# Kernel optimization log

Hardware: AMD Instinct MI355X
Metric: run time of the kernel (lower is better)

The kernel has to match this reference:

```python
import jax, jax.numpy as jnp
import numpy as np

BATCH, PAST_N, HID, FEAT = 256, 512, 512, 1
INIT_MULT = 0.01  # ones * 0.01 initial state (perturb_init=False / eval mode)


def setup_inputs() -> dict:
    key = jax.random.key(0)
    ks = jax.random.split(key, 8)
    s = 1.0 / np.sqrt(HID)
    return {
        "input_seq": jax.random.normal(ks[0], (BATCH, PAST_N, FEAT), dtype=jnp.float32),
        "future_n": 64,
        "W_ih": jax.random.uniform(ks[1], (4 * HID, FEAT), minval=-s, maxval=s, dtype=jnp.float32),
        "W_hh": jax.random.uniform(ks[2], (4 * HID, HID), minval=-s, maxval=s, dtype=jnp.float32),
        "b_ih": jax.random.uniform(ks[3], (4 * HID,), minval=-s, maxval=s, dtype=jnp.float32),
        "b_hh": jax.random.uniform(ks[4], (4 * HID,), minval=-s, maxval=s, dtype=jnp.float32),
        "W_dec": jax.random.uniform(ks[5], (FEAT, HID), minval=-s, maxval=s, dtype=jnp.float32),
        "b_dec": jax.random.uniform(ks[6], (FEAT,), minval=-s, maxval=s, dtype=jnp.float32),
    }


def _lstm_cell(x, h, c, W_ih, W_hh, b_ih, b_hh):
    # PyTorch LSTMCell: gates ordered (i, f, g, o)
    gates = x @ W_ih.T + b_ih + h @ W_hh.T + b_hh  # [B, 4H]
    i, f, g, o = jnp.split(gates, 4, axis=-1)
    c_new = jax.nn.sigmoid(f) * c + jax.nn.sigmoid(i) * jnp.tanh(g)
    h_new = jax.nn.sigmoid(o) * jnp.tanh(c_new)
    return h_new, c_new


def reference(input_seq, future_n, W_ih, W_hh, b_ih, b_hh, W_dec, b_dec):
    B, T, _ = input_seq.shape
    h0 = jnp.full((B, HID), INIT_MULT, dtype=input_seq.dtype)
    c0 = jnp.full((B, HID), INIT_MULT, dtype=input_seq.dtype)

    xs = jnp.swapaxes(input_seq, 0, 1)  # [T, B, F]

    def past_step(carry, x_t):
        h, c = carry
        h, c = _lstm_cell(x_t, h, c, W_ih, W_hh, b_ih, b_hh)
        return (h, c), h

    (h, c), past_h = jax.lax.scan(past_step, (h0, c0), xs)  # past_h: [T, B, H]

    def future_step(carry, _):
        h, c = carry
        x_t = h @ W_dec.T + b_dec  # decode hidden -> next input, [B, F]
        h, c = _lstm_cell(x_t, h, c, W_ih, W_hh, b_ih, b_hh)
        return (h, c), h

    _, fut_h = jax.lax.scan(future_step, (h, c), None, length=future_n)  # [F_n, B, H]

    all_h = jnp.concatenate([past_h, fut_h], axis=0)  # [T+F_n, B, H]
    all_h = jnp.swapaxes(all_h, 0, 1)  # [B, T+F_n, H]
    return all_h @ W_dec.T + b_dec  # [B, T+F_n, 1]
```

## Files before the change

kernel.cpp:

```cpp
#include <hip/hip_runtime.h>
#include <hip/hip_fp16.h>


#define TPAST 512
#define TTOT  576
#define HIDN  512
#define BW    16
#define HW    64
#define NGRP  8
#define NTHR  512
#define HSTR  520
#define HSTR64 130
#define GSTR  261
#define BATCHN 256

typedef _Float16 half8   __attribute__((ext_vector_type(8)));
typedef _Float16 half2v  __attribute__((ext_vector_type(2)));
typedef float    float4v __attribute__((ext_vector_type(4)));

__device__ __forceinline__ float fast_exp(float x) {
    return __builtin_amdgcn_exp2f(x * 1.44269504f);
}
__device__ __forceinline__ float fast_sigmoid(float x) {
    return __builtin_amdgcn_rcpf(1.0f + fast_exp(-x));
}
__device__ __forceinline__ float fast_tanh(float x) {
    return 1.0f - 2.0f * __builtin_amdgcn_rcpf(fast_exp(2.0f * x) + 1.0f);
}

__global__ __launch_bounds__(NTHR, 1)
void lstm_forecast_kernel(const float* __restrict__ xseq,
                          const float* __restrict__ Wih,
                          const float* __restrict__ Whh,
                          const float* __restrict__ bih,
                          const float* __restrict__ bhh,
                          const float* __restrict__ Wdec,
                          const float* __restrict__ bdec,
                          float* __restrict__ out,
                          unsigned int* __restrict__ flagbase,
                          unsigned int* __restrict__ hbuf)
{
    __shared__ _Float16 hcur[BW * HSTR];
    __shared__ float    gates[BW * GSTR];
    __shared__ float    wdecs[HIDN];
    __shared__ float    xcur[BW];

    const int tid  = threadIdx.x;
    const int bb   = blockIdx.x & 15;
    const int gb   = blockIdx.x >> 4;
    const int lane = tid & 63;
    const int wave = tid >> 6;
    const int m    = lane & 15;
    const int q    = lane >> 4;

    half8 Wf[2][16];
    {
        #pragma unroll
        for (int cbi = 0; cbi < 2; ++cbi) {
            const int col = (2 * wave + cbi) * 16 + m;
            const int gt  = col >> 6;
            const int jl  = col & 63;
            const float* wr = Whh + (size_t)(gt * HIDN + gb * HW + jl) * HIDN;
            #pragma unroll
            for (int kk = 0; kk < 16; ++kk) {
                const int k0 = kk * 32 + q * 8;
                float4v u = *(const float4v*)(wr + k0);
                float4v v = *(const float4v*)(wr + k0 + 4);
                half8 h;
                h[0] = (_Float16)u[0]; h[1] = (_Float16)u[1];
                h[2] = (_Float16)u[2]; h[3] = (_Float16)u[3];
                h[4] = (_Float16)v[0]; h[5] = (_Float16)v[1];
                h[6] = (_Float16)v[2]; h[7] = (_Float16)v[3];
                Wf[cbi][kk] = h;
            }
        }
    }

    const int eb = tid >> 5;
    const int jj = tid & 31;
    const int j0 = 2 * jj;
    float wih_r[2][4], bsum_r[2][4], wd[2];
    #pragma unroll
    for (int p = 0; p < 2; ++p) {
        const int jg = gb * HW + j0 + p;
        #pragma unroll
        for (int gt = 0; gt < 4; ++gt) {
            const int r = gt * HIDN + jg;
            wih_r[p][gt]  = Wih[r];
            bsum_r[p][gt] = bih[r] + bhh[r];
        }
        wd[p] = Wdec[jg];
    }
    const float bdecv = bdec[0];
    float c0 = 0.01f, c1 = 0.01f;

    {
        const _Float16 hinit = (_Float16)0.01f;
        for (int i = tid; i < BW * HSTR; i += NTHR) hcur[i] = hinit;
        wdecs[tid] = Wdec[tid];
        if (tid < BW) xcur[tid] = xseq[(bb * BW + tid) * TPAST + 0];
    }
    __syncthreads();

    unsigned int* gflags = flagbase + bb * 16;
    const int bglob_e = bb * BW + eb;
    const bool dp_lead = ((lane & 31) == 0);
    float dpv = 0.f;

    for (int t = 0; t < TTOT; ++t) {
        float4v acc0 = {0.f, 0.f, 0.f, 0.f};
        float4v acc1 = {0.f, 0.f, 0.f, 0.f};
        const _Float16* arow = hcur + m * HSTR + q * 8;
        #pragma unroll
        for (int kk = 0; kk < 16; ++kk) {
            half8 af = *(const half8*)(arow + kk * 32);
            acc0 = __builtin_amdgcn_mfma_f32_16x16x32_f16(af, Wf[0][kk], acc0, 0, 0, 0);
            acc1 = __builtin_amdgcn_mfma_f32_16x16x32_f16(af, Wf[1][kk], acc1, 0, 0, 0);
        }
        {
            const int colbase = wave * 32;
            #pragma unroll
            for (int r = 0; r < 4; ++r) {
                gates[(q * 4 + r) * GSTR + colbase +      m] = acc0[r];
                gates[(q * 4 + r) * GSTR + colbase + 16 + m] = acc1[r];
            }
        }
        const int tn = t + 1;
        float xq = 0.f;
        if (tn < TPAST && tid < BW) xq = xseq[(bb * BW + tid) * TPAST + tn];

        __syncthreads();

        {
            const float xc = xcur[eb];
            const float* grow = gates + eb * GSTR;

            float gi = grow[       j0] + xc * wih_r[0][0] + bsum_r[0][0];
            float gf = grow[ 64  + j0] + xc * wih_r[0][1] + bsum_r[0][1];
            float gg = grow[128  + j0] + xc * wih_r[0][2] + bsum_r[0][2];
            float go = grow[192  + j0] + xc * wih_r[0][3] + bsum_r[0][3];
            c0 = fast_sigmoid(gf) * c0 + fast_sigmoid(gi) * fast_tanh(gg);
            const float h0 = fast_sigmoid(go) * fast_tanh(c0);

            gi = grow[       j0 + 1] + xc * wih_r[1][0] + bsum_r[1][0];
            gf = grow[ 64  + j0 + 1] + xc * wih_r[1][1] + bsum_r[1][1];
            gg = grow[128  + j0 + 1] + xc * wih_r[1][2] + bsum_r[1][2];
            go = grow[192  + j0 + 1] + xc * wih_r[1][3] + bsum_r[1][3];
            c1 = fast_sigmoid(gf) * c1 + fast_sigmoid(gi) * fast_tanh(gg);
            const float h1 = fast_sigmoid(go) * fast_tanh(c1);

            half2v hp; hp[0] = (_Float16)h0; hp[1] = (_Float16)h1;
            const unsigned int bits = __builtin_bit_cast(unsigned int, hp);
            unsigned int* hdst = hbuf
                + (size_t)((tn & 1) * BATCHN + bglob_e) * (HIDN / 2)
                + gb * (HW / 2) + jj;
            __hip_atomic_store(hdst, bits, __ATOMIC_RELAXED,
                               __HIP_MEMORY_SCOPE_AGENT);

            float dp = h0 * wd[0] + h1 * wd[1];
            dp += __shfl_down(dp, 16);
            dp += __shfl_down(dp, 8);
            dp += __shfl_down(dp, 4);
            dp += __shfl_down(dp, 2);
            dp += __shfl_down(dp, 1);
            dpv = dp;
        }

        __syncthreads();

        if (t == TTOT - 1) {
            if (dp_lead)
                atomicAdd(out + bglob_e * TTOT + t,
                          dpv + (gb == 0 ? bdecv : 0.0f));
            break;
        }

        const unsigned int target = (unsigned int)tn;
        if (tid == 0)
            __hip_atomic_store(gflags + gb, target, __ATOMIC_RELAXED,
                               __HIP_MEMORY_SCOPE_AGENT);
        {
            const unsigned int* slot = gflags + (lane & 7);
            int guard = 0;
            for (;;) {
                const unsigned int v = __hip_atomic_load(
                    slot, __ATOMIC_RELAXED, __HIP_MEMORY_SCOPE_AGENT);
                if (__ballot(v >= target) == ~0ull) break;
                __builtin_amdgcn_s_sleep(1);
                if (++guard > (1 << 22)) break;
            }
        }
        __builtin_amdgcn_sched_barrier(0);

        {
            const int p1 = tn & 1;
            const unsigned long long* hsrc = (const unsigned long long*)hbuf
                + (size_t)(p1 * BATCHN + bb * BW) * (HIDN / 4);
            unsigned long long* hc64 = (unsigned long long*)hcur;
            #pragma unroll
            for (int i = 0; i < 4; ++i) {
                const int idx = lane + 64 * i;
                const int row = 2 * wave + (idx >> 7);
                const int col = idx & 127;
                hc64[row * HSTR64 + col] =
                    __hip_atomic_load(hsrc + row * (HIDN / 4) + col,
                                      __ATOMIC_RELAXED, __HIP_MEMORY_SCOPE_AGENT);
            }
        }
        __syncthreads();

        if (dp_lead)
            atomicAdd(out + bglob_e * TTOT + t,
                      dpv + (gb == 0 ? bdecv : 0.0f));
        if (tn >= TPAST) {
            const _Float16* hr = hcur + eb * HSTR + jj * 16;
            const float*    wr = wdecs + jj * 16;
            float dx = 0.f;
            #pragma unroll
            for (int u = 0; u < 2; ++u) {
                half8 hv = *(const half8*)(hr + u * 8);
                #pragma unroll
                for (int e = 0; e < 8; ++e)
                    dx += (float)hv[e] * wr[u * 8 + e];
            }
            dx += __shfl_down(dx, 16);
            dx += __shfl_down(dx, 8);
            dx += __shfl_down(dx, 4);
            dx += __shfl_down(dx, 2);
            dx += __shfl_down(dx, 1);
            if (dp_lead) xcur[eb] = dx + bdecv;
        } else {
            if (tid < BW) xcur[tid] = xq;
        }
    }
}

extern "C" void kernel_launch(void* const* d_in, const int* in_sizes, int n_in,
                              void* d_out, int out_size, void* d_ws, size_t ws_size,
                              hipStream_t stream) {
    (void)in_sizes; (void)n_in; (void)ws_size;
    const float* xseq = (const float*)d_in[0];
    const float* Wih  = (const float*)d_in[2];
    const float* Whh  = (const float*)d_in[3];
    const float* bih  = (const float*)d_in[4];
    const float* bhh  = (const float*)d_in[5];
    const float* Wdec = (const float*)d_in[6];
    const float* bdec = (const float*)d_in[7];
    float* out = (float*)d_out;

    unsigned int* flags = (unsigned int*)d_ws;
    unsigned int* hbuf  = (unsigned int*)((char*)d_ws + 8192);

    hipMemsetAsync(d_ws, 0, 8192, stream);
    hipMemsetAsync(d_out, 0, (size_t)out_size * sizeof(float), stream);
    lstm_forecast_kernel<<<dim3(128), dim3(NTHR), 0, stream>>>(
        xseq, Wih, Whh, bih, bhh, Wdec, bdec, out, flags, hbuf);
}
```

Before: 1.968 ms.

## Use sc0 cache-bypass loads/stores for inter-block sync with runtime validation

Replaces the agent-scope atomic loads and stores used for the cross-block hidden-state exchange and step flags with inline-asm global loads and stores carrying the sc0 bit. At startup each block group runs a token handshake to confirm that these accesses see each other's writes, and keeps the original atomic path as a fallback if any block fails. The aim is lower latency per recurrent step on the sync and h-exchange path. The cost is a one-time prologue handshake, an extra vmcnt drain before each step's barrier, and reliance on cache-coherence behaviour that the handshake checks at runtime rather than the memory model guaranteeing.

```diff
diff --git a/kernel.cpp b/kernel.cpp
--- a/kernel.cpp
+++ b/kernel.cpp
@@ -28,6 +28,29 @@
     return 1.0f - 2.0f * __builtin_amdgcn_rcpf(fast_exp(2.0f * x) + 1.0f);
 }
 
+__device__ __forceinline__ void st_sc0(unsigned int* p, unsigned int v) {
+    asm volatile("global_store_dword %0, %1, off sc0" :: "v"(p), "v"(v) : "memory");
+}
+__device__ __forceinline__ unsigned int ld_sc0(const unsigned int* p) {
+    unsigned int v;
+    asm volatile("global_load_dword %0, %1, off sc0\n\ts_waitcnt vmcnt(0)"
+                 : "=v"(v) : "v"(p) : "memory");
+    return v;
+}
+__device__ __forceinline__ void ld4_sc0(const unsigned long long* p,
+                                        unsigned long long& a, unsigned long long& b,
+                                        unsigned long long& c, unsigned long long& d) {
+    asm volatile("global_load_dwordx2 %0, %4, off sc0\n\t"
+                 "global_load_dwordx2 %1, %4, off offset:512 sc0\n\t"
+                 "global_load_dwordx2 %2, %4, off offset:1024 sc0\n\t"
+                 "global_load_dwordx2 %3, %4, off offset:1536 sc0\n\t"
+                 "s_waitcnt vmcnt(0)"
+                 : "=v"(a), "=v"(b), "=v"(c), "=v"(d) : "v"(p) : "memory");
+}
+__device__ __forceinline__ void drain_vm() {
+    asm volatile("s_waitcnt vmcnt(0)" ::: "memory");
+}
+
 __global__ __launch_bounds__(NTHR, 1)
 void lstm_forecast_kernel(const float* __restrict__ xseq,
                           const float* __restrict__ Wih,
@@ -37,13 +60,14 @@
                           const float* __restrict__ Wdec,
                           const float* __restrict__ bdec,
                           float* __restrict__ out,
-                          unsigned int* __restrict__ flagbase,
+                          unsigned int* __restrict__ ws32,
                           unsigned int* __restrict__ hbuf)
 {
     __shared__ _Float16 hcur[BW * HSTR];
     __shared__ float    gates[BW * GSTR];
     __shared__ float    wdecs[HIDN];
     __shared__ float    xcur[BW];
+    __shared__ int      vfast_s;
 
     const int tid  = threadIdx.x;
     const int bb   = blockIdx.x & 15;
@@ -52,6 +76,11 @@
     const int wave = tid >> 6;
     const int m    = lane & 15;
     const int q    = lane >> 4;
+
+    unsigned int* gflags  = ws32 + bb * 16;
+    unsigned int* vflags  = ws32 + 1024 / 4 + bb * 16;
+    unsigned int* okflags = ws32 + 2048 / 4 + bb * 16;
+    unsigned int* tokens  = ws32 + 3072 / 4;
 
     half8 Wf[2][16];
     {
@@ -100,9 +129,57 @@
         wdecs[tid] = Wdec[tid];
         if (tid < BW) xcur[tid] = xseq[(bb * BW + tid) * TPAST + 0];
     }
+
+    if (wave == 0) {
+        unsigned int okacc = 1;
+        for (int r = 0; r < 3; ++r) {
+            if (lane == 0) {
+                st_sc0(tokens + (bb * 8 + gb) * 16, (unsigned)(r * 16 + gb + 1));
+                drain_vm();
+                __hip_atomic_store(vflags + gb, (unsigned)(r + 1),
+                                   __ATOMIC_RELAXED, __HIP_MEMORY_SCOPE_AGENT);
+            }
+            {
+                int guard = 0;
+                for (;;) {
+                    unsigned int v = (lane < 8)
+                        ? __hip_atomic_load(vflags + lane, __ATOMIC_RELAXED,
+                                            __HIP_MEMORY_SCOPE_AGENT)
+                        : 0xFFFFFFFFu;
+                    if (__ballot(v >= (unsigned)(r + 1)) == ~0ull) break;
+                    __builtin_amdgcn_s_sleep(1);
+                    if (++guard > (1 << 20)) { okacc = 0; break; }
+                }
+            }
+            unsigned int tv = 0;
+            if (lane < 8) tv = ld_sc0(tokens + (bb * 8 + lane) * 16);
+            const bool mine = (lane >= 8) || (tv == (unsigned)(r * 16 + lane + 1));
+            if (__ballot(mine) != ~0ull) okacc = 0;
+        }
+        if (lane == 0)
+            __hip_atomic_store(okflags + gb, okacc + 1u,
+                               __ATOMIC_RELAXED, __HIP_MEMORY_SCOPE_AGENT);
+        unsigned int allfast = 0;
+        {
+            int guard = 0;
+            for (;;) {
+                unsigned int v = (lane < 8)
+                    ? __hip_atomic_load(okflags + lane, __ATOMIC_RELAXED,
+                                        __HIP_MEMORY_SCOPE_AGENT)
+                    : 1u;
+                if (__ballot(v != 0) == ~0ull) {
+                    allfast = (__ballot(v == 2u || lane >= 8) == ~0ull) ? 1u : 0u;
+                    break;
+                }
+                __builtin_amdgcn_s_sleep(1);
+                if (++guard > (1 << 20)) { allfast = 0; break; }
+            }
+        }
+        if (lane == 0) vfast_s = (int)allfast;
+    }
     __syncthreads();
-
-    unsigned int* gflags = flagbase + bb * 16;
+    const bool vfast = (vfast_s != 0);
+
     const int bglob_e = bb * BW + eb;
     const bool dp_lead = ((lane & 31) == 0);
     float dpv = 0.f;
@@ -154,8 +231,11 @@
             unsigned int* hdst = hbuf
                 + (size_t)((tn & 1) * BATCHN + bglob_e) * (HIDN / 2)
                 + gb * (HW / 2) + jj;
-            __hip_atomic_store(hdst, bits, __ATOMIC_RELAXED,
-                               __HIP_MEMORY_SCOPE_AGENT);
+            if (vfast)
+                st_sc0(hdst, bits);
+            else
+                __hip_atomic_store(hdst, bits, __ATOMIC_RELAXED,
+                                   __HIP_MEMORY_SCOPE_AGENT);
 
             float dp = h0 * wd[0] + h1 * wd[1];
             dp += __shfl_down(dp, 16);
@@ -166,6 +246,7 @@
             dpv = dp;
         }
 
+        drain_vm();
         __syncthreads();
 
         if (t == TTOT - 1) {
@@ -176,18 +257,29 @@
         }
 
         const unsigned int target = (unsigned int)tn;
-        if (tid == 0)
-            __hip_atomic_store(gflags + gb, target, __ATOMIC_RELAXED,
-                               __HIP_MEMORY_SCOPE_AGENT);
+        if (tid == 0) {
+            if (vfast) st_sc0(gflags + gb, target);
+            else __hip_atomic_store(gflags + gb, target, __ATOMIC_RELAXED,
+                                    __HIP_MEMORY_SCOPE_AGENT);
+        }
         {
             const unsigned int* slot = gflags + (lane & 7);
             int guard = 0;
-            for (;;) {
-                const unsigned int v = __hip_atomic_load(
-                    slot, __ATOMIC_RELAXED, __HIP_MEMORY_SCOPE_AGENT);
-                if (__ballot(v >= target) == ~0ull) break;
-                __builtin_amdgcn_s_sleep(1);
-                if (++guard > (1 << 22)) break;
+            if (vfast) {
+                for (;;) {
+                    const unsigned int v = ld_sc0(slot);
+                    if (__ballot(v >= target) == ~0ull) break;
+                    __builtin_amdgcn_s_sleep(1);
+                    if (++guard > (1 << 16)) break;
+                }
+            } else {
+                for (;;) {
+                    const unsigned int v = __hip_atomic_load(
+                        slot, __ATOMIC_RELAXED, __HIP_MEMORY_SCOPE_AGENT);
+                    if (__ballot(v >= target) == ~0ull) break;
+                    __builtin_amdgcn_s_sleep(1);
+                    if (++guard > (1 << 22)) break;
+                }
             }
         }
         __builtin_amdgcn_sched_barrier(0);
@@ -197,14 +289,24 @@
             const unsigned long long* hsrc = (const unsigned long long*)hbuf
                 + (size_t)(p1 * BATCHN + bb * BW) * (HIDN / 4);
             unsigned long long* hc64 = (unsigned long long*)hcur;
-            #pragma unroll
-            for (int i = 0; i < 4; ++i) {
-                const int idx = lane + 64 * i;
-                const int row = 2 * wave + (idx >> 7);
-                const int col = idx & 127;
-                hc64[row * HSTR64 + col] =
-                    __hip_atomic_load(hsrc + row * (HIDN / 4) + col,
-                                      __ATOMIC_RELAXED, __HIP_MEMORY_SCOPE_AGENT);
+            if (vfast) {
+                const unsigned long long* base = hsrc + (2 * wave) * 128 + lane;
+                unsigned long long d0, d1, d2, d3;
+                ld4_sc0(base, d0, d1, d2, d3);
+                hc64[(2 * wave    ) * HSTR64 + lane     ] = d0;
+                hc64[(2 * wave    ) * HSTR64 + lane + 64] = d1;
+                hc64[(2 * wave + 1) * HSTR64 + lane     ] = d2;
+                hc64[(2 * wave + 1) * HSTR64 + lane + 64] = d3;
+            } else {
+                #pragma unroll
+                for (int i = 0; i < 4; ++i) {
+                    const int idx = lane + 64 * i;
+                    const int row = 2 * wave + (idx >> 7);
+                    const int col = idx & 127;
+                    hc64[row * HSTR64 + col] =
+                        __hip_atomic_load(hsrc + row * (HIDN / 4) + col,
+                                          __ATOMIC_RELAXED, __HIP_MEMORY_SCOPE_AGENT);
+                }
             }
         }
         __syncthreads();
@@ -248,11 +350,11 @@
     const float* bdec = (const float*)d_in[7];
     float* out = (float*)d_out;
 
-    unsigned int* flags = (unsigned int*)d_ws;
-    unsigned int* hbuf  = (unsigned int*)((char*)d_ws + 8192);
-
-    hipMemsetAsync(d_ws, 0, 8192, stream);
+    unsigned int* ws32 = (unsigned int*)d_ws;
+    unsigned int* hbuf = (unsigned int*)((char*)d_ws + 65536);
+
+    hipMemsetAsync(d_ws, 0, 65536, stream);
     hipMemsetAsync(d_out, 0, (size_t)out_size * sizeof(float), stream);
     lstm_forecast_kernel<<<dim3(128), dim3(NTHR), 0, stream>>>(
-        xseq, Wih, Whh, bih, bhh, Wdec, bdec, out, flags, hbuf);
-}
+        xseq, Wih, Whh, bih, bhh, Wdec, bdec, out, ws32, hbuf);
+}
```

Measured after the change: 2.684 ms. 1.36x slower.

## Compute output decode from the gathered hidden state instead of atomic partial sums

Applied to the files above, without the earlier changes.

Each workgroup no longer computes a partial decoder dot product over its 64 hidden units and atomically adds it into the output. Instead, after the full hidden-state exchange, waves 0–1 each compute the complete decode for one batch row and write it with a plain store, which also removes the output memset. The hidden-state gather now uses inline-asm 32-byte dwordx4 loads with sc0/sc1 cache bits, and an explicit vmcnt drain is added before the barrier. The trade-offs: the final timestep now waits on one extra exchange, and the cache-bypassing loads may cost more latency per step.

```diff
diff --git a/kernel.cpp b/kernel.cpp
--- a/kernel.cpp
+++ b/kernel.cpp
@@ -8,15 +8,16 @@
 #define BW    16
 #define HW    64
 #define NGRP  8
+#define NWG   128
 #define NTHR  512
 #define HSTR  520
-#define HSTR64 130
 #define GSTR  261
 #define BATCHN 256
 
 typedef _Float16 half8   __attribute__((ext_vector_type(8)));
 typedef _Float16 half2v  __attribute__((ext_vector_type(2)));
 typedef float    float4v __attribute__((ext_vector_type(4)));
+typedef int      int4v   __attribute__((ext_vector_type(4)));
 
 __device__ __forceinline__ float fast_exp(float x) {
     return __builtin_amdgcn_exp2f(x * 1.44269504f);
@@ -26,6 +27,16 @@
 }
 __device__ __forceinline__ float fast_tanh(float x) {
     return 1.0f - 2.0f * __builtin_amdgcn_rcpf(fast_exp(2.0f * x) + 1.0f);
+}
+
+__device__ __forceinline__ void ld32_sys(const void* p, int4v& a, int4v& b) {
+    asm volatile("global_load_dwordx4 %0, %2, off sc0 sc1\n\t"
+                 "global_load_dwordx4 %1, %2, off offset:16 sc0 sc1\n\t"
+                 "s_waitcnt vmcnt(0)"
+                 : "=v"(a), "=v"(b) : "v"(p) : "memory");
+}
+__device__ __forceinline__ void drain_vm() {
+    asm volatile("s_waitcnt vmcnt(0)" ::: "memory");
 }
 
 __global__ __launch_bounds__(NTHR, 1)
@@ -79,7 +90,7 @@
     const int eb = tid >> 5;
     const int jj = tid & 31;
     const int j0 = 2 * jj;
-    float wih_r[2][4], bsum_r[2][4], wd[2];
+    float wih_r[2][4], bsum_r[2][4];
     #pragma unroll
     for (int p = 0; p < 2; ++p) {
         const int jg = gb * HW + j0 + p;
@@ -89,7 +100,6 @@
             wih_r[p][gt]  = Wih[r];
             bsum_r[p][gt] = bih[r] + bhh[r];
         }
-        wd[p] = Wdec[jg];
     }
     const float bdecv = bdec[0];
     float c0 = 0.01f, c1 = 0.01f;
@@ -104,8 +114,6 @@
 
     unsigned int* gflags = flagbase + bb * 16;
     const int bglob_e = bb * BW + eb;
-    const bool dp_lead = ((lane & 31) == 0);
-    float dpv = 0.f;
 
     for (int t = 0; t < TTOT; ++t) {
         float4v acc0 = {0.f, 0.f, 0.f, 0.f};
@@ -156,24 +164,10 @@
                 + gb * (HW / 2) + jj;
             __hip_atomic_store(hdst, bits, __ATOMIC_RELAXED,
                                __HIP_MEMORY_SCOPE_AGENT);
-
-            float dp = h0 * wd[0] + h1 * wd[1];
-            dp += __shfl_down(dp, 16);
-            dp += __shfl_down(dp, 8);
-            dp += __shfl_down(dp, 4);
-            dp += __shfl_down(dp, 2);
-            dp += __shfl_down(dp, 1);
-            dpv = dp;
-        }
-
+        }
+
+        drain_vm();
         __syncthreads();
-
-        if (t == TTOT - 1) {
-            if (dp_lead)
-                atomicAdd(out + bglob_e * TTOT + t,
-                          dpv + (gb == 0 ? bdecv : 0.0f));
-            break;
-        }
 
         const unsigned int target = (unsigned int)tn;
         if (tid == 0)
@@ -194,24 +188,35 @@
 
         {
             const int p1 = tn & 1;
-            const unsigned long long* hsrc = (const unsigned long long*)hbuf
-                + (size_t)(p1 * BATCHN + bb * BW) * (HIDN / 4);
-            unsigned long long* hc64 = (unsigned long long*)hcur;
-            #pragma unroll
-            for (int i = 0; i < 4; ++i) {
-                const int idx = lane + 64 * i;
-                const int row = 2 * wave + (idx >> 7);
-                const int col = idx & 127;
-                hc64[row * HSTR64 + col] =
-                    __hip_atomic_load(hsrc + row * (HIDN / 4) + col,
-                                      __ATOMIC_RELAXED, __HIP_MEMORY_SCOPE_AGENT);
-            }
+            const char* hsrc = (const char*)hbuf
+                + ((size_t)(p1 * BATCHN + bb * BW)) * (HIDN * 2);
+            const int row = 2 * wave + (lane >> 5);
+            const int cb  = (lane & 31) * 32;
+            int4v a, b;
+            ld32_sys(hsrc + row * (HIDN * 2) + cb, a, b);
+            _Float16* dst = hcur + row * HSTR + (lane & 31) * 16;
+            *(int4v*)(dst)     = a;
+            *(int4v*)(dst + 8) = b;
         }
         __syncthreads();
 
-        if (dp_lead)
-            atomicAdd(out + bglob_e * TTOT + t,
-                      dpv + (gb == 0 ? bdecv : 0.0f));
+        if (wave < 2) {
+            const int brow = 2 * gb + wave;
+            const _Float16* hr = hcur + brow * HSTR + lane * 8;
+            const float*    wr = wdecs + lane * 8;
+            half8 hv = *(const half8*)hr;
+            float dx = 0.f;
+            #pragma unroll
+            for (int e = 0; e < 8; ++e) dx += (float)hv[e] * wr[e];
+            dx += __shfl_down(dx, 32);
+            dx += __shfl_down(dx, 16);
+            dx += __shfl_down(dx, 8);
+            dx += __shfl_down(dx, 4);
+            dx += __shfl_down(dx, 2);
+            dx += __shfl_down(dx, 1);
+            if (lane == 0)
+                out[(bb * BW + brow) * TTOT + t] = dx + bdecv;
+        }
         if (tn >= TPAST) {
             const _Float16* hr = hcur + eb * HSTR + jj * 16;
             const float*    wr = wdecs + jj * 16;
@@ -228,7 +233,7 @@
             dx += __shfl_down(dx, 4);
             dx += __shfl_down(dx, 2);
             dx += __shfl_down(dx, 1);
-            if (dp_lead) xcur[eb] = dx + bdecv;
+            if ((lane & 31) == 0) xcur[eb] = dx + bdecv;
         } else {
             if (tid < BW) xcur[tid] = xq;
         }
@@ -238,7 +243,7 @@
 extern "C" void kernel_launch(void* const* d_in, const int* in_sizes, int n_in,
                               void* d_out, int out_size, void* d_ws, size_t ws_size,
                               hipStream_t stream) {
-    (void)in_sizes; (void)n_in; (void)ws_size;
+    (void)in_sizes; (void)n_in; (void)ws_size; (void)out_size;
     const float* xseq = (const float*)d_in[0];
     const float* Wih  = (const float*)d_in[2];
     const float* Whh  = (const float*)d_in[3];
@@ -252,7 +257,6 @@
     unsigned int* hbuf  = (unsigned int*)((char*)d_ws + 8192);
 
     hipMemsetAsync(d_ws, 0, 8192, stream);
-    hipMemsetAsync(d_out, 0, (size_t)out_size * sizeof(float), stream);
-    lstm_forecast_kernel<<<dim3(128), dim3(NTHR), 0, stream>>>(
+    lstm_forecast_kernel<<<dim3(NWG), dim3(NTHR), 0, stream>>>(
         xseq, Wih, Whh, bih, bhh, Wdec, bdec, out, flags, hbuf);
 }
```

After: 1.662 ms. 1.18x faster.
